# Performance work log

Measured on AMD Instinct MI355X. Metric: run time of the kernel, lower is better.

The kernel has to match this reference:

```python
import jax, jax.numpy as jnp
import numpy as np

IN_DIMS = 1024
K = 8


def setup_inputs() -> dict:
    key = jax.random.key(0)
    ks = jax.random.split(key, 7)
    s = 1.0 / np.sqrt(IN_DIMS)
    x = jax.random.normal(ks[0], (8, 2048, IN_DIMS), dtype=jnp.float32)
    Wq = jax.random.uniform(ks[1], (IN_DIMS, K), jnp.float32, -s, s)
    bq = jax.random.uniform(ks[2], (K,), jnp.float32, -s, s)
    Wk = jax.random.uniform(ks[3], (IN_DIMS, K), jnp.float32, -s, s)
    bk = jax.random.uniform(ks[4], (K,), jnp.float32, -s, s)
    Wv = jax.random.uniform(ks[5], (IN_DIMS, IN_DIMS), jnp.float32, -s, s)
    bv = jax.random.uniform(ks[6], (IN_DIMS,), jnp.float32, -s, s)
    return {"x": x, "Wq": Wq, "bq": bq, "Wk": Wk, "bk": bk, "Wv": Wv, "bv": bv}


def reference(x, Wq, bq, Wk, bk, Wv, bv):
    # x: [B,S,D]; rank-k projections
    q = jnp.einsum('bsd,dk->bsk', x, Wq) + bq        # [B,S,k]
    k = jnp.einsum('bsd,dk->bsk', x, Wk) + bk        # [B,S,k]
    energy = jnp.einsum('bik,bjk->bij', q, k)        # [B,S,S] (unscaled)
    attention = jax.nn.softmax(energy, axis=-1)
    value = jnp.einsum('bsd,de->bse', x, Wv) + bv    # [B,S,D]
    out = jnp.einsum('bij,bjd->bid', attention, value)
    return (out, attention)
```

## Files before the change

### kernel.cpp

```cpp
#include <hip/hip_runtime.h>


typedef __attribute__((ext_vector_type(8))) __bf16 bf16x8;
typedef __attribute__((ext_vector_type(4))) __bf16 bf16x4;
typedef __attribute__((ext_vector_type(4))) float  f32x4;
typedef unsigned int u32;

#define GLB_CAST(p) ((const __attribute__((address_space(1))) u32*)(p))
#define LDS_CAST(p) ((__attribute__((address_space(3))) u32*)(p))

#define S_BARRIER() { __builtin_amdgcn_s_barrier(); __builtin_amdgcn_sched_barrier(0); }
#define LGKM0()     { asm volatile("s_waitcnt lgkmcnt(0)" ::: "memory"); __builtin_amdgcn_sched_barrier(0); }
#define VMCNT8()    { asm volatile("s_waitcnt vmcnt(8)" ::: "memory"); __builtin_amdgcn_sched_barrier(0); }
#define VMCNT0()    { asm volatile("s_waitcnt vmcnt(0)" ::: "memory"); __builtin_amdgcn_sched_barrier(0); }

static constexpr int    Bn   = 8;
static constexpr int    S    = 2048;
static constexpr int    Dd   = 1024;
static constexpr int    Mtot = Bn * S;
static constexpr size_t OUT0 = (size_t)Bn * S * Dd;

static constexpr size_t OFF_XBF  = 0;
static constexpr size_t OFF_WVT  = OFF_XBF  + (size_t)Mtot * Dd * 2;
static constexpr size_t OFF_WQKT = OFF_WVT  + (size_t)Dd * Dd * 2;
static constexpr size_t OFF_Q    = OFF_WQKT + (size_t)16 * Dd * 2;
static constexpr size_t OFF_K    = OFF_Q    + (size_t)Mtot * 8 * 4;
static constexpr size_t OFF_VT   = OFF_K    + (size_t)Mtot * 8 * 4;
static constexpr size_t OFF_ATTB = OFF_VT   + (size_t)Bn * Dd * S * 2;
static constexpr size_t WS_NEED  = OFF_ATTB + (size_t)Bn * S * S * 2;

__global__ __launch_bounds__(256) void prep_kernel(
    const float* __restrict__ x, const float* __restrict__ Wq,
    const float* __restrict__ Wk, const float* __restrict__ Wv,
    __bf16* __restrict__ xbf, __bf16* __restrict__ wvt, __bf16* __restrict__ wqkT)
{
    __shared__ float lt[64][65];
    int bid = blockIdx.x, t = threadIdx.x;
    if (bid < 4096) {
        #pragma unroll
        for (int i = 0; i < 4; ++i) {
            size_t idx4 = (size_t)i * 1048576 + (size_t)bid * 256 + t;
            f32x4 v = ((const f32x4*)x)[idx4];
            bf16x4 o;
            #pragma unroll
            for (int c = 0; c < 4; ++c) o[c] = (__bf16)v[c];
            ((bf16x4*)xbf)[idx4] = o;
        }
    } else if (bid < 4352) {
        int tile = bid - 4096;
        int tr = tile >> 4, tc = tile & 15;
        int r0 = t >> 6, c = t & 63;
        #pragma unroll
        for (int i = 0; i < 16; ++i) {
            int row = i * 4 + r0;
            lt[row][c] = Wv[(size_t)(tr * 64 + row) * 1024 + tc * 64 + c];
        }
        __syncthreads();
        #pragma unroll
        for (int i = 0; i < 16; ++i) {
            int er = i * 4 + r0;
            wvt[(size_t)(tc * 64 + er) * 1024 + tr * 64 + c] = (__bf16)lt[c][er];
        }
    } else {
        int lb = bid - 4352;
        #pragma unroll
        for (int i = 0; i < 4; ++i) {
            int idx = (lb * 4 + i) * 256 + t;
            int n = idx >> 10, d = idx & 1023;
            float v = (n < 8) ? Wq[d * 8 + n] : Wk[d * 8 + (n & 7)];
            wqkT[n * 1024 + d] = (__bf16)v;
        }
    }
}

__global__ __launch_bounds__(256) void qk_proj_kernel(
    const __bf16* __restrict__ xbf, const __bf16* __restrict__ wqkT,
    const float* __restrict__ bq, const float* __restrict__ bk,
    float* __restrict__ qb, float* __restrict__ kb)
{
    int t = threadIdx.x, l = t & 63, w = t >> 6;
    int mbase = (blockIdx.x * 4 + w) * 16;
    f32x4 acc = {0.f, 0.f, 0.f, 0.f};
    const __bf16* ar = xbf + (size_t)(mbase + (l & 15)) * 1024 + ((l >> 4) << 3);
    const __bf16* br = wqkT + (size_t)(l & 15) * 1024 + ((l >> 4) << 3);
    #pragma unroll 8
    for (int kk = 0; kk < 1024; kk += 32) {
        bf16x8 a = *(const bf16x8*)(ar + kk);
        bf16x8 b = *(const bf16x8*)(br + kk);
        acc = __builtin_amdgcn_mfma_f32_16x16x32_bf16(a, b, acc, 0, 0, 0);
    }
    int n = l & 15;
    float bias = (n < 8) ? bq[n] : bk[n & 7];
    #pragma unroll
    for (int r = 0; r < 4; ++r) {
        int m = mbase + ((l >> 4) << 2) + r;
        float v = acc[r] + bias;
        if (n < 8) qb[m * 8 + n] = v;
        else       kb[m * 8 + (n & 7)] = v;
    }
}

__global__ __launch_bounds__(256) void softmax_kernel(
    const float* __restrict__ qb, const float* __restrict__ kb,
    float* __restrict__ attnF, __bf16* __restrict__ attnB)
{
    int bid = blockIdx.x;
    int b = bid >> 6, chunk = bid & 63;
    int t = threadIdx.x, l = t & 63, w = t >> 6;
    float kr[8][8];
    const float* kbb = kb + ((size_t)b << 14);
    #pragma unroll
    for (int jj = 0; jj < 8; ++jj) {
        f32x4 v0 = *(const f32x4*)(kbb + (size_t)(t * 8 + jj) * 8);
        f32x4 v1 = *(const f32x4*)(kbb + (size_t)(t * 8 + jj) * 8 + 4);
        #pragma unroll
        for (int c = 0; c < 4; ++c) { kr[jj][c] = v0[c]; kr[jj][4 + c] = v1[c]; }
    }
    __shared__ float redm[4], reds[4];
    const float* qrow = qb + ((size_t)b << 14);
    for (int ii = 0; ii < 32; ++ii) {
        int i = (chunk << 5) + ii;
        f32x4 q0 = *(const f32x4*)(qrow + (size_t)i * 8);
        f32x4 q1 = *(const f32x4*)(qrow + (size_t)i * 8 + 4);
        float e[8];
        #pragma unroll
        for (int jj = 0; jj < 8; ++jj) {
            float s = q0[0] * kr[jj][0];
            s = fmaf(q0[1], kr[jj][1], s);
            s = fmaf(q0[2], kr[jj][2], s);
            s = fmaf(q0[3], kr[jj][3], s);
            s = fmaf(q1[0], kr[jj][4], s);
            s = fmaf(q1[1], kr[jj][5], s);
            s = fmaf(q1[2], kr[jj][6], s);
            s = fmaf(q1[3], kr[jj][7], s);
            e[jj] = s;
        }
        float mx = e[0];
        #pragma unroll
        for (int jj = 1; jj < 8; ++jj) mx = fmaxf(mx, e[jj]);
        #pragma unroll
        for (int d = 1; d < 64; d <<= 1) mx = fmaxf(mx, __shfl_xor(mx, d));
        if (l == 0) redm[w] = mx;
        __syncthreads();
        mx = fmaxf(fmaxf(redm[0], redm[1]), fmaxf(redm[2], redm[3]));
        float p[8], sum = 0.f;
        #pragma unroll
        for (int jj = 0; jj < 8; ++jj) { p[jj] = __expf(e[jj] - mx); sum += p[jj]; }
        #pragma unroll
        for (int d = 1; d < 64; d <<= 1) sum += __shfl_xor(sum, d);
        if (l == 0) reds[w] = sum;
        __syncthreads();
        float T = (reds[0] + reds[1]) + (reds[2] + reds[3]);
        float inv = 1.0f / T;
        size_t off = (((size_t)b << 11) + i) * 2048 + (size_t)t * 8;
        f32x4 o0, o1; bf16x8 ob;
        #pragma unroll
        for (int c = 0; c < 4; ++c) {
            o0[c] = p[c] * inv; o1[c] = p[4 + c] * inv;
            ob[c] = (__bf16)o0[c]; ob[4 + c] = (__bf16)o1[c];
        }
        *(f32x4*)(attnF + off) = o0;
        *(f32x4*)(attnF + off + 4) = o1;
        *(bf16x8*)(attnB + off) = ob;
    }
}

template<int LDA>
__device__ __forceinline__ void stageA(const __bf16* Ab, char* smem,
    int slot, int kk, int c, int rowin, int sl8, int wid)
{
    __builtin_amdgcn_global_load_lds(
        GLB_CAST(Ab + (size_t)(c * 64 + rowin) * LDA + kk + sl8 * 8),
        LDS_CAST(smem + slot * 65536 + c * 8192 + wid * 1024), 16, 0, 0);
}
template<int LDA>
__device__ __forceinline__ void stageB(const __bf16* Bb, char* smem,
    int slot, int kk, int c, int rowin, int sl8, int wid)
{
    __builtin_amdgcn_global_load_lds(
        GLB_CAST(Bb + (size_t)(c * 64 + rowin) * LDA + kk + sl8 * 8),
        LDS_CAST(smem + slot * 65536 + 32768 + c * 8192 + wid * 1024), 16, 0, 0);
}

template<int MODE>
__global__ __launch_bounds__(512, 2) void gemm_kernel(
    const __bf16* __restrict__ A, const __bf16* __restrict__ Bt,
    float* __restrict__ outF, __bf16* __restrict__ outVt,
    const float* __restrict__ bv)
{
    constexpr int LDA = (MODE == 0) ? 1024 : 2048;
    constexpr int NT  = LDA / 64;
    __shared__ __align__(1024) char smem[131072];

    int bid = blockIdx.x;
    int wg = ((bid & 7) << 5) | (bid >> 3);
    int t = threadIdx.x, l = t & 63;
    int wid = t >> 6;
    int wmr = wid >> 2, wnc = wid & 3;

    int mblk, nblk, bb = 0;
    size_t aoff, boff;
    if constexpr (MODE == 0) {
        mblk = wg >> 2; nblk = wg & 3;
        aoff = (size_t)mblk * 256 * LDA; boff = 0;
    } else {
        bb = wg >> 5; int r = wg & 31;
        mblk = r >> 2; nblk = r & 3;
        aoff = (size_t)bb * S * S + (size_t)mblk * 256 * LDA;
        boff = (size_t)bb * Dd * S;
    }
    const __bf16* Ab = A + aoff;
    const __bf16* Bb = Bt + boff + (size_t)nblk * 256 * LDA;

    int rowin = t >> 3;
    int sl8 = (t & 7) ^ (rowin & 7);
    int lr = l & 15, lk = l >> 4;

    f32x4 acc[8][4] = {};

    #pragma unroll
    for (int c = 0; c < 4; ++c) {
        stageA<LDA>(Ab, smem, 0, 0, c, rowin, sl8, wid);
        stageB<LDA>(Bb, smem, 0, 0, c, rowin, sl8, wid);
    }
    #pragma unroll
    for (int c = 0; c < 4; ++c) {
        stageA<LDA>(Ab, smem, 1, 64, c, rowin, sl8, wid);
        stageB<LDA>(Bb, smem, 1, 64, c, rowin, sl8, wid);
    }
    VMCNT8();
    S_BARRIER();

    for (int tt = 0; tt < NT; ++tt) {
        int s = tt & 1;
        const __bf16* Asl = (const __bf16*)(smem + s * 65536);
        const __bf16* Bsl = (const __bf16*)(smem + s * 65536 + 32768);
        bool pf = (tt + 2 < NT);
        int kk2 = (tt + 2) * 64;

        bf16x8 aLo[2][4], aHi[2][4], bLo[2][2], bHi[2][2];

        #pragma unroll
        for (int ks = 0; ks < 2; ++ks) {
            int sa = ks * 4 + lk;
            #pragma unroll
            for (int i = 0; i < 4; ++i) {
                int ra = wmr * 128 + i * 16 + lr;
                aLo[ks][i] = *(const bf16x8*)&Asl[ra * 64 + ((sa ^ (ra & 7)) << 3)];
            }
            #pragma unroll
            for (int j = 0; j < 2; ++j) {
                int rb = wnc * 64 + j * 16 + lr;
                bLo[ks][j] = *(const bf16x8*)&Bsl[rb * 64 + ((sa ^ (rb & 7)) << 3)];
            }
        }
        S_BARRIER(); LGKM0();
        __builtin_amdgcn_s_setprio(1);
        #pragma unroll
        for (int ks = 0; ks < 2; ++ks)
            #pragma unroll
            for (int i = 0; i < 4; ++i)
                #pragma unroll
                for (int j = 0; j < 2; ++j)
                    acc[i][j] = __builtin_amdgcn_mfma_f32_16x16x32_bf16(aLo[ks][i], bLo[ks][j], acc[i][j], 0, 0, 0);
        __builtin_amdgcn_s_setprio(0);
        S_BARRIER();

        #pragma unroll
        for (int ks = 0; ks < 2; ++ks) {
            int sa = ks * 4 + lk;
            #pragma unroll
            for (int j = 0; j < 2; ++j) {
                int rb = wnc * 64 + (j + 2) * 16 + lr;
                bHi[ks][j] = *(const bf16x8*)&Bsl[rb * 64 + ((sa ^ (rb & 7)) << 3)];
            }
        }
        if (pf) {
            stageA<LDA>(Ab, smem, s, kk2, 0, rowin, sl8, wid);
            stageA<LDA>(Ab, smem, s, kk2, 2, rowin, sl8, wid);
        }
        S_BARRIER(); LGKM0();
        __builtin_amdgcn_s_setprio(1);
        #pragma unroll
        for (int ks = 0; ks < 2; ++ks)
            #pragma unroll
            for (int i = 0; i < 4; ++i)
                #pragma unroll
                for (int j = 0; j < 2; ++j)
                    acc[i][2 + j] = __builtin_amdgcn_mfma_f32_16x16x32_bf16(aLo[ks][i], bHi[ks][j], acc[i][2 + j], 0, 0, 0);
        __builtin_amdgcn_s_setprio(0);
        S_BARRIER();

        #pragma unroll
        for (int ks = 0; ks < 2; ++ks) {
            int sa = ks * 4 + lk;
            #pragma unroll
            for (int i = 0; i < 4; ++i) {
                int ra = wmr * 128 + (i + 4) * 16 + lr;
                aHi[ks][i] = *(const bf16x8*)&Asl[ra * 64 + ((sa ^ (ra & 7)) << 3)];
            }
        }
        if (pf) {
            #pragma unroll
            for (int c = 0; c < 4; ++c)
                stageB<LDA>(Bb, smem, s, kk2, c, rowin, sl8, wid);
        }
        S_BARRIER(); LGKM0();
        __builtin_amdgcn_s_setprio(1);
        #pragma unroll
        for (int ks = 0; ks < 2; ++ks)
            #pragma unroll
            for (int i = 0; i < 4; ++i)
                #pragma unroll
                for (int j = 0; j < 2; ++j)
                    acc[4 + i][2 + j] = __builtin_amdgcn_mfma_f32_16x16x32_bf16(aHi[ks][i], bHi[ks][j], acc[4 + i][2 + j], 0, 0, 0);
        __builtin_amdgcn_s_setprio(0);
        S_BARRIER();

        if (pf) {
            stageA<LDA>(Ab, smem, s, kk2, 1, rowin, sl8, wid);
            stageA<LDA>(Ab, smem, s, kk2, 3, rowin, sl8, wid);
        }
        S_BARRIER();
        __builtin_amdgcn_s_setprio(1);
        #pragma unroll
        for (int ks = 0; ks < 2; ++ks)
            #pragma unroll
            for (int i = 0; i < 4; ++i)
                #pragma unroll
                for (int j = 0; j < 2; ++j)
                    acc[4 + i][j] = __builtin_amdgcn_mfma_f32_16x16x32_bf16(aHi[ks][i], bLo[ks][j], acc[4 + i][j], 0, 0, 0);
        __builtin_amdgcn_s_setprio(0);

        if (tt == NT - 1) break;
        S_BARRIER();
        if (pf) { VMCNT8(); } else { VMCNT0(); }
        S_BARRIER();
    }

    if constexpr (MODE == 0) {
        #pragma unroll
        for (int j = 0; j < 4; ++j) {
            int e = (nblk << 8) + wnc * 64 + j * 16 + lr;
            float bias = bv[e];
            #pragma unroll
            for (int i = 0; i < 8; ++i) {
                int m0 = (mblk << 8) + wmr * 128 + i * 16 + (lk << 2);
                int b = m0 >> 11, s0 = m0 & 2047;
                bf16x4 o;
                #pragma unroll
                for (int r = 0; r < 4; ++r) o[r] = (__bf16)(acc[i][j][r] + bias);
                *(bf16x4*)&outVt[(((size_t)(b << 10) + e) << 11) + s0] = o;
            }
        }
    } else {
        float* ob = outF + (size_t)bb * S * Dd;
        #pragma unroll
        for (int i = 0; i < 8; ++i) {
            int m0 = (mblk << 8) + wmr * 128 + i * 16 + (lk << 2);
            #pragma unroll
            for (int j = 0; j < 4; ++j) {
                int e = (nblk << 8) + wnc * 64 + j * 16 + lr;
                #pragma unroll
                for (int r = 0; r < 4; ++r)
                    ob[(size_t)(m0 + r) * 1024 + e] = acc[i][j][r];
            }
        }
    }
}

extern "C" void kernel_launch(void* const* d_in, const int* in_sizes, int n_in,
                              void* d_out, int out_size, void* d_ws, size_t ws_size,
                              hipStream_t stream)
{
    const float* x  = (const float*)d_in[0];
    const float* Wq = (const float*)d_in[1];
    const float* bq = (const float*)d_in[2];
    const float* Wk = (const float*)d_in[3];
    const float* bk = (const float*)d_in[4];
    const float* Wv = (const float*)d_in[5];
    const float* bv = (const float*)d_in[6];

    float* outp  = (float*)d_out;
    float* attnF = outp + OUT0;

    if (ws_size < WS_NEED) return;
    char* ws = (char*)d_ws;
    __bf16* xbf   = (__bf16*)(ws + OFF_XBF);
    __bf16* wvt   = (__bf16*)(ws + OFF_WVT);
    __bf16* wqkT  = (__bf16*)(ws + OFF_WQKT);
    float*  qbuf  = (float*)(ws + OFF_Q);
    float*  kbuf  = (float*)(ws + OFF_K);
    __bf16* vt    = (__bf16*)(ws + OFF_VT);
    __bf16* attnB = (__bf16*)(ws + OFF_ATTB);

    prep_kernel<<<4368, 256, 0, stream>>>(x, Wq, Wk, Wv, xbf, wvt, wqkT);
    qk_proj_kernel<<<256, 256, 0, stream>>>(xbf, wqkT, bq, bk, qbuf, kbuf);
    gemm_kernel<0><<<256, 512, 0, stream>>>(xbf, wvt, nullptr, vt, bv);
    softmax_kernel<<<512, 256, 0, stream>>>(qbuf, kbuf, attnF, attnB);
    gemm_kernel<1><<<256, 512, 0, stream>>>(attnB, vt, outp, nullptr, nullptr);
}
```

Before: 196.3 us.

## Fuse softmax recomputation into attention-times-value GEMM, dropping bf16 attention buffer

The softmax kernel now writes only each row's max and reciprocal sum. A new fused kernel recomputes the rank-8 energies tile by tile, applies exp and normalisation, writes the fp32 attention output (from one of the two column-half blocks), and feeds bf16 probabilities through LDS into MFMA against staged V tiles. This removes the 64MB bf16 attention write and its re-read by the second GEMM. The cost is a second exp pass over the energies, a smaller tile GEMM with less reuse per block, and per-tile barriers.

```diff
diff --git a/kernel.cpp b/kernel.cpp
--- a/kernel.cpp
+++ b/kernel.cpp
@@ -12,6 +12,7 @@
 #define S_BARRIER() { __builtin_amdgcn_s_barrier(); __builtin_amdgcn_sched_barrier(0); }
 #define LGKM0()     { asm volatile("s_waitcnt lgkmcnt(0)" ::: "memory"); __builtin_amdgcn_sched_barrier(0); }
 #define VMCNT8()    { asm volatile("s_waitcnt vmcnt(8)" ::: "memory"); __builtin_amdgcn_sched_barrier(0); }
+#define VMCNT4()    { asm volatile("s_waitcnt vmcnt(4)" ::: "memory"); __builtin_amdgcn_sched_barrier(0); }
 #define VMCNT0()    { asm volatile("s_waitcnt vmcnt(0)" ::: "memory"); __builtin_amdgcn_sched_barrier(0); }
 
 static constexpr int    Bn   = 8;
@@ -26,8 +27,9 @@
 static constexpr size_t OFF_Q    = OFF_WQKT + (size_t)16 * Dd * 2;
 static constexpr size_t OFF_K    = OFF_Q    + (size_t)Mtot * 8 * 4;
 static constexpr size_t OFF_VT   = OFF_K    + (size_t)Mtot * 8 * 4;
-static constexpr size_t OFF_ATTB = OFF_VT   + (size_t)Bn * Dd * S * 2;
-static constexpr size_t WS_NEED  = OFF_ATTB + (size_t)Bn * S * S * 2;
+static constexpr size_t OFF_M    = OFF_VT   + (size_t)Bn * Dd * S * 2;
+static constexpr size_t OFF_T    = OFF_M    + (size_t)Mtot * 4;
+static constexpr size_t WS_NEED  = OFF_T    + (size_t)Mtot * 4;
 
 __global__ __launch_bounds__(256) void prep_kernel(
     const float* __restrict__ x, const float* __restrict__ Wq,
@@ -100,9 +102,9 @@
     }
 }
 
-__global__ __launch_bounds__(256) void softmax_kernel(
+__global__ __launch_bounds__(256) void mt_kernel(
     const float* __restrict__ qb, const float* __restrict__ kb,
-    float* __restrict__ attnF, __bf16* __restrict__ attnB)
+    float* __restrict__ mArr, float* __restrict__ tArr)
 {
     int bid = blockIdx.x;
     int b = bid >> 6, chunk = bid & 63;
@@ -143,25 +145,19 @@
         if (l == 0) redm[w] = mx;
         __syncthreads();
         mx = fmaxf(fmaxf(redm[0], redm[1]), fmaxf(redm[2], redm[3]));
-        float p[8], sum = 0.f;
-        #pragma unroll
-        for (int jj = 0; jj < 8; ++jj) { p[jj] = __expf(e[jj] - mx); sum += p[jj]; }
+        float sum = 0.f;
+        #pragma unroll
+        for (int jj = 0; jj < 8; ++jj) sum += __expf(e[jj] - mx);
         #pragma unroll
         for (int d = 1; d < 64; d <<= 1) sum += __shfl_xor(sum, d);
         if (l == 0) reds[w] = sum;
         __syncthreads();
         float T = (reds[0] + reds[1]) + (reds[2] + reds[3]);
-        float inv = 1.0f / T;
-        size_t off = (((size_t)b << 11) + i) * 2048 + (size_t)t * 8;
-        f32x4 o0, o1; bf16x8 ob;
-        #pragma unroll
-        for (int c = 0; c < 4; ++c) {
-            o0[c] = p[c] * inv; o1[c] = p[4 + c] * inv;
-            ob[c] = (__bf16)o0[c]; ob[4 + c] = (__bf16)o1[c];
-        }
-        *(f32x4*)(attnF + off) = o0;
-        *(f32x4*)(attnF + off + 4) = o1;
-        *(bf16x8*)(attnB + off) = ob;
+        if (t == 0) {
+            mArr[(b << 11) + i] = mx;
+            tArr[(b << 11) + i] = 1.0f / T;
+        }
+        __syncthreads();
     }
 }
 
@@ -182,13 +178,11 @@
         LDS_CAST(smem + slot * 65536 + 32768 + c * 8192 + wid * 1024), 16, 0, 0);
 }
 
-template<int MODE>
-__global__ __launch_bounds__(512, 2) void gemm_kernel(
+__global__ __launch_bounds__(512, 2) void gemm0_kernel(
     const __bf16* __restrict__ A, const __bf16* __restrict__ Bt,
-    float* __restrict__ outF, __bf16* __restrict__ outVt,
-    const float* __restrict__ bv)
-{
-    constexpr int LDA = (MODE == 0) ? 1024 : 2048;
+    __bf16* __restrict__ outVt, const float* __restrict__ bv)
+{
+    constexpr int LDA = 1024;
     constexpr int NT  = LDA / 64;
     __shared__ __align__(1024) char smem[131072];
 
@@ -198,19 +192,9 @@
     int wid = t >> 6;
     int wmr = wid >> 2, wnc = wid & 3;
 
-    int mblk, nblk, bb = 0;
-    size_t aoff, boff;
-    if constexpr (MODE == 0) {
-        mblk = wg >> 2; nblk = wg & 3;
-        aoff = (size_t)mblk * 256 * LDA; boff = 0;
-    } else {
-        bb = wg >> 5; int r = wg & 31;
-        mblk = r >> 2; nblk = r & 3;
-        aoff = (size_t)bb * S * S + (size_t)mblk * 256 * LDA;
-        boff = (size_t)bb * Dd * S;
-    }
-    const __bf16* Ab = A + aoff;
-    const __bf16* Bb = Bt + boff + (size_t)nblk * 256 * LDA;
+    int mblk = wg >> 2, nblk = wg & 3;
+    const __bf16* Ab = A + (size_t)mblk * 256 * LDA;
+    const __bf16* Bb = Bt + (size_t)nblk * 256 * LDA;
 
     int rowin = t >> 3;
     int sl8 = (t & 7) ^ (rowin & 7);
@@ -338,33 +322,144 @@
         S_BARRIER();
     }
 
-    if constexpr (MODE == 0) {
-        #pragma unroll
-        for (int j = 0; j < 4; ++j) {
-            int e = (nblk << 8) + wnc * 64 + j * 16 + lr;
-            float bias = bv[e];
-            #pragma unroll
-            for (int i = 0; i < 8; ++i) {
-                int m0 = (mblk << 8) + wmr * 128 + i * 16 + (lk << 2);
-                int b = m0 >> 11, s0 = m0 & 2047;
-                bf16x4 o;
-                #pragma unroll
-                for (int r = 0; r < 4; ++r) o[r] = (__bf16)(acc[i][j][r] + bias);
-                *(bf16x4*)&outVt[(((size_t)(b << 10) + e) << 11) + s0] = o;
-            }
-        }
-    } else {
-        float* ob = outF + (size_t)bb * S * Dd;
+    #pragma unroll
+    for (int j = 0; j < 4; ++j) {
+        int e = (nblk << 8) + wnc * 64 + j * 16 + lr;
+        float bias = bv[e];
         #pragma unroll
         for (int i = 0; i < 8; ++i) {
             int m0 = (mblk << 8) + wmr * 128 + i * 16 + (lk << 2);
-            #pragma unroll
-            for (int j = 0; j < 4; ++j) {
-                int e = (nblk << 8) + wnc * 64 + j * 16 + lr;
-                #pragma unroll
-                for (int r = 0; r < 4; ++r)
-                    ob[(size_t)(m0 + r) * 1024 + e] = acc[i][j][r];
-            }
+            int b = m0 >> 11, s0 = m0 & 2047;
+            bf16x4 o;
+            #pragma unroll
+            for (int r = 0; r < 4; ++r) o[r] = (__bf16)(acc[i][j][r] + bias);
+            *(bf16x4*)&outVt[(((size_t)(b << 10) + e) << 11) + s0] = o;
+        }
+    }
+}
+
+__device__ __forceinline__ void stageV(const __bf16* vtb, char* smem, int vs,
+    int jt0, int t, int wid)
+{
+    #pragma unroll
+    for (int u = 0; u < 4; ++u) {
+        int el = u * 128 + (t >> 2);
+        int sc = (t & 3) ^ ((el >> 1) & 3);
+        __builtin_amdgcn_global_load_lds(
+            GLB_CAST(vtb + (size_t)el * 2048 + jt0 + sc * 8),
+            LDS_CAST(smem + vs * 32768 + u * 8192 + wid * 1024), 16, 0, 0);
+    }
+}
+
+__device__ __forceinline__ void pcompute(int jt0, int ps, char* smem,
+    const float* kbb, f32x4 q0, f32x4 q1, float m, float invT,
+    float* aF, bool writeA, int pr, int jg)
+{
+    float p[8];
+    const float* kp = kbb + (size_t)(jt0 + jg * 8) * 8;
+    #pragma unroll
+    for (int jj = 0; jj < 8; ++jj) {
+        f32x4 k0 = *(const f32x4*)(kp + jj * 8);
+        f32x4 k1 = *(const f32x4*)(kp + jj * 8 + 4);
+        float s = q0[0] * k0[0];
+        s = fmaf(q0[1], k0[1], s);
+        s = fmaf(q0[2], k0[2], s);
+        s = fmaf(q0[3], k0[3], s);
+        s = fmaf(q1[0], k1[0], s);
+        s = fmaf(q1[1], k1[1], s);
+        s = fmaf(q1[2], k1[2], s);
+        s = fmaf(q1[3], k1[3], s);
+        p[jj] = __expf(s - m) * invT;
+    }
+    if (writeA) {
+        f32x4 o0 = {p[0], p[1], p[2], p[3]};
+        f32x4 o1 = {p[4], p[5], p[6], p[7]};
+        *(f32x4*)(aF + jt0 + jg * 8) = o0;
+        *(f32x4*)(aF + jt0 + jg * 8 + 4) = o1;
+    }
+    bf16x8 pb;
+    #pragma unroll
+    for (int c = 0; c < 8; ++c) pb[c] = (__bf16)p[c];
+    int sl = jg ^ ((pr >> 1) & 3);
+    *(bf16x8*)(smem + 65536 + ps * 8192 + pr * 64 + (sl << 4)) = pb;
+}
+
+__global__ __launch_bounds__(512, 2) void fused_pv_kernel(
+    const float* __restrict__ qb, const float* __restrict__ kb,
+    const float* __restrict__ mArr, const float* __restrict__ tArr,
+    const __bf16* __restrict__ vt, float* __restrict__ attnF,
+    float* __restrict__ outp)
+{
+    __shared__ __align__(1024) char smem[81920];
+    int bid = blockIdx.x;
+    int b = bid & 7, rr = bid >> 3;
+    int itile = rr >> 1, nh = rr & 1;
+    int i0 = itile * 128, e0 = nh * 512;
+    int t = threadIdx.x, l = t & 63, wid = t >> 6;
+    int lr = l & 15, lk = l >> 4;
+
+    int pr = t >> 2, jg = t & 3;
+    int grow = (b << 11) + i0 + pr;
+    const float* qrow = qb + (size_t)grow * 8;
+    f32x4 q0 = *(const f32x4*)(qrow);
+    f32x4 q1 = *(const f32x4*)(qrow + 4);
+    float m    = mArr[grow];
+    float invT = tArr[grow];
+    const float* kbb = kb + ((size_t)b << 14);
+    const __bf16* vtb = vt + (((size_t)(b << 10) + e0) << 11);
+    float* aF = attnF + ((size_t)grow << 11);
+    bool writeA = (nh == 0);
+
+    f32x4 acc[8][4] = {};
+
+    pcompute(0, 0, smem, kbb, q0, q1, m, invT, aF, writeA, pr, jg);
+    stageV(vtb, smem, 0, 0, t, wid);
+    VMCNT0(); LGKM0();
+    S_BARRIER();
+
+    for (int tt = 0; tt < 64; ++tt) {
+        int s = tt & 1;
+        if (tt < 63) {
+            pcompute((tt + 1) * 32, s ^ 1, smem, kbb, q0, q1, m, invT, aF, writeA, pr, jg);
+            stageV(vtb, smem, s ^ 1, (tt + 1) * 32, t, wid);
+            VMCNT4();
+        } else {
+            VMCNT0();
+        }
+        LGKM0();
+        S_BARRIER();
+
+        const char* Vs = smem + s * 32768;
+        const char* Ps = smem + 65536 + s * 8192;
+        bf16x8 bfr[4];
+        #pragma unroll
+        for (int eb = 0; eb < 4; ++eb) {
+            int el = wid * 64 + eb * 16 + lr;
+            bfr[eb] = *(const bf16x8*)(Vs + el * 64 + ((lk ^ ((el >> 1) & 3)) << 4));
+        }
+        __builtin_amdgcn_s_setprio(1);
+        #pragma unroll
+        for (int i = 0; i < 8; ++i) {
+            int row = i * 16 + lr;
+            bf16x8 af = *(const bf16x8*)(Ps + row * 64 + ((lk ^ ((row >> 1) & 3)) << 4));
+            #pragma unroll
+            for (int eb = 0; eb < 4; ++eb)
+                acc[i][eb] = __builtin_amdgcn_mfma_f32_16x16x32_bf16(af, bfr[eb], acc[i][eb], 0, 0, 0);
+        }
+        __builtin_amdgcn_s_setprio(0);
+        S_BARRIER();
+    }
+
+    float* ob = outp + ((size_t)b << 21);
+    #pragma unroll
+    for (int i = 0; i < 8; ++i) {
+        int m0 = i0 + i * 16 + (lk << 2);
+        #pragma unroll
+        for (int eb = 0; eb < 4; ++eb) {
+            int e = e0 + wid * 64 + eb * 16 + lr;
+            #pragma unroll
+            for (int r = 0; r < 4; ++r)
+                ob[(size_t)(m0 + r) * 1024 + e] = acc[i][eb][r];
         }
     }
 }
@@ -392,11 +487,12 @@
     float*  qbuf  = (float*)(ws + OFF_Q);
     float*  kbuf  = (float*)(ws + OFF_K);
     __bf16* vt    = (__bf16*)(ws + OFF_VT);
-    __bf16* attnB = (__bf16*)(ws + OFF_ATTB);
+    float*  mArr  = (float*)(ws + OFF_M);
+    float*  tArr  = (float*)(ws + OFF_T);
 
     prep_kernel<<<4368, 256, 0, stream>>>(x, Wq, Wk, Wv, xbf, wvt, wqkT);
     qk_proj_kernel<<<256, 256, 0, stream>>>(xbf, wqkT, bq, bk, qbuf, kbuf);
-    gemm_kernel<0><<<256, 512, 0, stream>>>(xbf, wvt, nullptr, vt, bv);
-    softmax_kernel<<<512, 256, 0, stream>>>(qbuf, kbuf, attnF, attnB);
-    gemm_kernel<1><<<256, 512, 0, stream>>>(attnB, vt, outp, nullptr, nullptr);
-}
+    mt_kernel<<<512, 256, 0, stream>>>(qbuf, kbuf, mArr, tArr);
+    gemm0_kernel<<<256, 512, 0, stream>>>(xbf, wvt, vt, bv);
+    fused_pv_kernel<<<256, 512, 0, stream>>>(qbuf, kbuf, mArr, tArr, vt, attnF, outp);
+}
```

Result: slower. 433.5 us (+120.8%).

## Fuse x bf16 conversion into Q/K projection and V GEMM, drop xbf buffer

Applied to the files above, without the earlier changes.

Removes the separate pass that converted x to a bf16 workspace copy. The Q/K projection now reads fp32 x directly inside the prep kernel, and a new dedicated V GEMM kernel loads fp32 x into registers, converts it and writes swizzled bf16 tiles to LDS with a two-stage prefetch. The V^T output is also transposed through LDS so that global stores are 16-byte contiguous. This cuts a full write and re-read of a bf16 copy of x and one kernel launch. In exchange the V GEMM reads twice as many bytes for A and does the conversion in its main loop, and its pipeline uses register loads with full vmcnt(0) waits instead of async LDS loads.

```diff
diff --git a/kernel.cpp b/kernel.cpp
--- a/kernel.cpp
+++ b/kernel.cpp
@@ -20,34 +20,50 @@
 static constexpr int    Mtot = Bn * S;
 static constexpr size_t OUT0 = (size_t)Bn * S * Dd;
 
-static constexpr size_t OFF_XBF  = 0;
-static constexpr size_t OFF_WVT  = OFF_XBF  + (size_t)Mtot * Dd * 2;
-static constexpr size_t OFF_WQKT = OFF_WVT  + (size_t)Dd * Dd * 2;
-static constexpr size_t OFF_Q    = OFF_WQKT + (size_t)16 * Dd * 2;
-static constexpr size_t OFF_K    = OFF_Q    + (size_t)Mtot * 8 * 4;
-static constexpr size_t OFF_VT   = OFF_K    + (size_t)Mtot * 8 * 4;
-static constexpr size_t OFF_ATTB = OFF_VT   + (size_t)Bn * Dd * S * 2;
+static constexpr size_t OFF_WVT  = 0;
+static constexpr size_t OFF_Q    = OFF_WVT + (size_t)Dd * Dd * 2;
+static constexpr size_t OFF_K    = OFF_Q   + (size_t)Mtot * 8 * 4;
+static constexpr size_t OFF_VT   = OFF_K   + (size_t)Mtot * 8 * 4;
+static constexpr size_t OFF_ATTB = OFF_VT  + (size_t)Bn * Dd * S * 2;
 static constexpr size_t WS_NEED  = OFF_ATTB + (size_t)Bn * S * S * 2;
 
 __global__ __launch_bounds__(256) void prep_kernel(
     const float* __restrict__ x, const float* __restrict__ Wq,
     const float* __restrict__ Wk, const float* __restrict__ Wv,
-    __bf16* __restrict__ xbf, __bf16* __restrict__ wvt, __bf16* __restrict__ wqkT)
+    const float* __restrict__ bq, const float* __restrict__ bk,
+    __bf16* __restrict__ wvt, float* __restrict__ qb, float* __restrict__ kb)
 {
     __shared__ float lt[64][65];
     int bid = blockIdx.x, t = threadIdx.x;
-    if (bid < 4096) {
-        #pragma unroll
-        for (int i = 0; i < 4; ++i) {
-            size_t idx4 = (size_t)i * 1048576 + (size_t)bid * 256 + t;
-            f32x4 v = ((const f32x4*)x)[idx4];
-            bf16x4 o;
-            #pragma unroll
-            for (int c = 0; c < 4; ++c) o[c] = (__bf16)v[c];
-            ((bf16x4*)xbf)[idx4] = o;
-        }
-    } else if (bid < 4352) {
-        int tile = bid - 4096;
+    if (bid < 256) {
+        int l = t & 63, w = t >> 6;
+        int mbase = (bid * 4 + w) * 16;
+        int n = l & 15;
+        int dbase = (l >> 4) << 3;
+        const float* xr = x + (size_t)(mbase + n) * 1024 + dbase;
+        const float* wcol = (n < 8) ? (Wq + n) : (Wk + (n & 7));
+        f32x4 acc = {0.f, 0.f, 0.f, 0.f};
+        #pragma unroll 4
+        for (int kk = 0; kk < 1024; kk += 32) {
+            f32x4 a0 = *(const f32x4*)(xr + kk);
+            f32x4 a1 = *(const f32x4*)(xr + kk + 4);
+            bf16x8 a, b;
+            #pragma unroll
+            for (int c = 0; c < 4; ++c) { a[c] = (__bf16)a0[c]; a[4 + c] = (__bf16)a1[c]; }
+            #pragma unroll
+            for (int u = 0; u < 8; ++u) b[u] = (__bf16)wcol[(size_t)(dbase + kk + u) * 8];
+            acc = __builtin_amdgcn_mfma_f32_16x16x32_bf16(a, b, acc, 0, 0, 0);
+        }
+        float bias = (n < 8) ? bq[n] : bk[n & 7];
+        #pragma unroll
+        for (int r = 0; r < 4; ++r) {
+            int m = mbase + ((l >> 4) << 2) + r;
+            float v = acc[r] + bias;
+            if (n < 8) qb[m * 8 + n] = v;
+            else       kb[m * 8 + (n & 7)] = v;
+        }
+    } else {
+        int tile = bid - 256;
         int tr = tile >> 4, tc = tile & 15;
         int r0 = t >> 6, c = t & 63;
         #pragma unroll
@@ -61,42 +77,165 @@
             int er = i * 4 + r0;
             wvt[(size_t)(tc * 64 + er) * 1024 + tr * 64 + c] = (__bf16)lt[c][er];
         }
-    } else {
-        int lb = bid - 4352;
-        #pragma unroll
-        for (int i = 0; i < 4; ++i) {
-            int idx = (lb * 4 + i) * 256 + t;
-            int n = idx >> 10, d = idx & 1023;
-            float v = (n < 8) ? Wq[d * 8 + n] : Wk[d * 8 + (n & 7)];
-            wqkT[n * 1024 + d] = (__bf16)v;
-        }
-    }
-}
-
-__global__ __launch_bounds__(256) void qk_proj_kernel(
-    const __bf16* __restrict__ xbf, const __bf16* __restrict__ wqkT,
-    const float* __restrict__ bq, const float* __restrict__ bk,
-    float* __restrict__ qb, float* __restrict__ kb)
-{
-    int t = threadIdx.x, l = t & 63, w = t >> 6;
-    int mbase = (blockIdx.x * 4 + w) * 16;
-    f32x4 acc = {0.f, 0.f, 0.f, 0.f};
-    const __bf16* ar = xbf + (size_t)(mbase + (l & 15)) * 1024 + ((l >> 4) << 3);
-    const __bf16* br = wqkT + (size_t)(l & 15) * 1024 + ((l >> 4) << 3);
-    #pragma unroll 8
-    for (int kk = 0; kk < 1024; kk += 32) {
-        bf16x8 a = *(const bf16x8*)(ar + kk);
-        bf16x8 b = *(const bf16x8*)(br + kk);
-        acc = __builtin_amdgcn_mfma_f32_16x16x32_bf16(a, b, acc, 0, 0, 0);
-    }
-    int n = l & 15;
-    float bias = (n < 8) ? bq[n] : bk[n & 7];
-    #pragma unroll
-    for (int r = 0; r < 4; ++r) {
-        int m = mbase + ((l >> 4) << 2) + r;
-        float v = acc[r] + bias;
-        if (n < 8) qb[m * 8 + n] = v;
-        else       kb[m * 8 + (n & 7)] = v;
+    }
+}
+
+__global__ __launch_bounds__(512, 2) void gemm0_kernel(
+    const float* __restrict__ X, const __bf16* __restrict__ Wvt,
+    __bf16* __restrict__ outVt, const float* __restrict__ bv)
+{
+    constexpr int NT = 16;
+    __shared__ __align__(1024) char smem[131072];
+
+    int bid = blockIdx.x;
+    int wg = ((bid & 7) << 5) | (bid >> 3);
+    int t = threadIdx.x, l = t & 63, wid = t >> 6;
+    int wmr = wid >> 2, wnc = wid & 3;
+    int mblk = wg >> 2, nblk = wg & 3;
+
+    int arow = t >> 1, ahalf = t & 1;
+    const float* Ax = X + (size_t)(mblk * 256 + arow) * 1024 + ahalf * 32;
+    int awoff[4];
+    #pragma unroll
+    for (int u = 0; u < 4; ++u)
+        awoff[u] = arow * 128 + (((ahalf * 4 + u) ^ (arow & 7)) << 4);
+
+    int rowin = t >> 3;
+    int sl8 = (t & 7) ^ (rowin & 7);
+    const __bf16* gB[4];
+    #pragma unroll
+    for (int c = 0; c < 4; ++c)
+        gB[c] = Wvt + (size_t)(nblk * 256 + c * 64 + rowin) * 1024 + sl8 * 8;
+
+    int lr = l & 15, lk = l >> 4;
+    int slot0 = (lk ^ (lr & 7)) << 3;
+    int slot1 = ((lk ^ 4) ^ (lr & 7)) << 3;
+    int offA0 = (wmr * 128 + lr) * 64 + slot0;
+    int offA1 = (wmr * 128 + lr) * 64 + slot1;
+    int offB0 = (wnc * 64 + lr) * 64 + slot0;
+    int offB1 = (wnc * 64 + lr) * 64 + slot1;
+
+    f32x4 acc[8][4] = {};
+    f32x4 xr[8];
+
+    #pragma unroll
+    for (int i = 0; i < 8; ++i) xr[i] = *(const f32x4*)(Ax + 0 * 64 + i * 4);
+    VMCNT0();
+    #pragma unroll
+    for (int u = 0; u < 4; ++u) {
+        f32x4 a0 = xr[2 * u], a1 = xr[2 * u + 1];
+        bf16x8 wv_;
+        #pragma unroll
+        for (int c = 0; c < 4; ++c) { wv_[c] = (__bf16)a0[c]; wv_[4 + c] = (__bf16)a1[c]; }
+        *(bf16x8*)(smem + awoff[u]) = wv_;
+    }
+    #pragma unroll
+    for (int c = 0; c < 4; ++c)
+        __builtin_amdgcn_global_load_lds(GLB_CAST(gB[c] + 0),
+            LDS_CAST(smem + 32768 + c * 8192 + wid * 1024), 16, 0, 0);
+    #pragma unroll
+    for (int i = 0; i < 8; ++i) xr[i] = *(const f32x4*)(Ax + 1 * 64 + i * 4);
+    VMCNT0();
+    #pragma unroll
+    for (int u = 0; u < 4; ++u) {
+        f32x4 a0 = xr[2 * u], a1 = xr[2 * u + 1];
+        bf16x8 wv_;
+        #pragma unroll
+        for (int c = 0; c < 4; ++c) { wv_[c] = (__bf16)a0[c]; wv_[4 + c] = (__bf16)a1[c]; }
+        *(bf16x8*)(smem + 65536 + awoff[u]) = wv_;
+    }
+    #pragma unroll
+    for (int c = 0; c < 4; ++c)
+        __builtin_amdgcn_global_load_lds(GLB_CAST(gB[c] + 64),
+            LDS_CAST(smem + 65536 + 32768 + c * 8192 + wid * 1024), 16, 0, 0);
+    VMCNT0();
+    LGKM0();
+    S_BARRIER();
+
+    for (int tt = 0; tt < NT; ++tt) {
+        bool pf = (tt + 2 < NT);
+        if (pf) {
+            #pragma unroll
+            for (int i = 0; i < 8; ++i)
+                xr[i] = *(const f32x4*)(Ax + (tt + 2) * 64 + i * 4);
+            __builtin_amdgcn_sched_barrier(0);
+        }
+        const __bf16* Asl = (const __bf16*)(smem + ((tt & 1) << 16));
+        const __bf16* Bsl = Asl + 16384;
+        bf16x8 af[8], bfr[4];
+        #pragma unroll
+        for (int i = 0; i < 8; ++i) af[i] = *(const bf16x8*)(Asl + offA0 + i * 1024);
+        #pragma unroll
+        for (int j = 0; j < 4; ++j) bfr[j] = *(const bf16x8*)(Bsl + offB0 + j * 1024);
+        __builtin_amdgcn_s_setprio(1);
+        #pragma unroll
+        for (int i = 0; i < 8; ++i)
+            #pragma unroll
+            for (int j = 0; j < 4; ++j)
+                acc[i][j] = __builtin_amdgcn_mfma_f32_16x16x32_bf16(af[i], bfr[j], acc[i][j], 0, 0, 0);
+        __builtin_amdgcn_s_setprio(0);
+        #pragma unroll
+        for (int i = 0; i < 8; ++i) af[i] = *(const bf16x8*)(Asl + offA1 + i * 1024);
+        #pragma unroll
+        for (int j = 0; j < 4; ++j) bfr[j] = *(const bf16x8*)(Bsl + offB1 + j * 1024);
+        __builtin_amdgcn_s_setprio(1);
+        #pragma unroll
+        for (int i = 0; i < 8; ++i)
+            #pragma unroll
+            for (int j = 0; j < 4; ++j)
+                acc[i][j] = __builtin_amdgcn_mfma_f32_16x16x32_bf16(af[i], bfr[j], acc[i][j], 0, 0, 0);
+        __builtin_amdgcn_s_setprio(0);
+
+        if (tt == NT - 1) break;
+        S_BARRIER();
+        VMCNT0();
+        if (pf) {
+            char* dst = smem + ((tt & 1) << 16);
+            #pragma unroll
+            for (int u = 0; u < 4; ++u) {
+                f32x4 a0 = xr[2 * u], a1 = xr[2 * u + 1];
+                bf16x8 wv_;
+                #pragma unroll
+                for (int c = 0; c < 4; ++c) { wv_[c] = (__bf16)a0[c]; wv_[4 + c] = (__bf16)a1[c]; }
+                *(bf16x8*)(dst + awoff[u]) = wv_;
+            }
+            #pragma unroll
+            for (int c = 0; c < 4; ++c)
+                __builtin_amdgcn_global_load_lds(GLB_CAST(gB[c] + (tt + 2) * 64),
+                    LDS_CAST(dst + 32768 + c * 8192 + wid * 1024), 16, 0, 0);
+            LGKM0();
+        }
+        S_BARRIER();
+    }
+
+    S_BARRIER();
+    #pragma unroll
+    for (int j = 0; j < 4; ++j) {
+        int e_loc = wnc * 64 + j * 16 + lr;
+        float bias = bv[(nblk << 8) + e_loc];
+        #pragma unroll
+        for (int i = 0; i < 8; ++i) {
+            int slot = wmr * 16 + i * 2 + (lk >> 1);
+            bf16x4 o;
+            #pragma unroll
+            for (int r = 0; r < 4; ++r) o[r] = (__bf16)(acc[i][j][r] + bias);
+            *(bf16x4*)(smem + e_loc * 512 + ((slot ^ (e_loc & 7)) << 4) + (lk & 1) * 8) = o;
+        }
+    }
+    S_BARRIER();
+    int b = mblk >> 3, sbase = (mblk & 7) << 8;
+    #pragma unroll
+    for (int u = 0; u < 4; ++u) {
+        int e_loc = u * 64 + (t >> 3);
+        int e_glob = (nblk << 8) + e_loc;
+        __bf16* dstp = outVt + (((size_t)(b << 10) + e_glob) << 11) + sbase;
+        int sv = t & 7;
+        #pragma unroll
+        for (int v = 0; v < 4; ++v) {
+            int svv = v * 8 + sv;
+            bf16x8 val = *(const bf16x8*)(smem + e_loc * 512 + ((svv ^ (e_loc & 7)) << 4));
+            *(bf16x8*)(dstp + svv * 8) = val;
+        }
     }
 }
 
@@ -165,31 +304,26 @@
     }
 }
 
-template<int LDA>
-__device__ __forceinline__ void stageA(const __bf16* Ab, char* smem,
+__device__ __forceinline__ void g1_stageA(const __bf16* Ab, char* smem,
     int slot, int kk, int c, int rowin, int sl8, int wid)
 {
     __builtin_amdgcn_global_load_lds(
-        GLB_CAST(Ab + (size_t)(c * 64 + rowin) * LDA + kk + sl8 * 8),
+        GLB_CAST(Ab + (size_t)(c * 64 + rowin) * 2048 + kk + sl8 * 8),
         LDS_CAST(smem + slot * 65536 + c * 8192 + wid * 1024), 16, 0, 0);
 }
-template<int LDA>
-__device__ __forceinline__ void stageB(const __bf16* Bb, char* smem,
+__device__ __forceinline__ void g1_stageB(const __bf16* Bb, char* smem,
     int slot, int kk, int c, int rowin, int sl8, int wid)
 {
     __builtin_amdgcn_global_load_lds(
-        GLB_CAST(Bb + (size_t)(c * 64 + rowin) * LDA + kk + sl8 * 8),
+        GLB_CAST(Bb + (size_t)(c * 64 + rowin) * 2048 + kk + sl8 * 8),
         LDS_CAST(smem + slot * 65536 + 32768 + c * 8192 + wid * 1024), 16, 0, 0);
 }
 
-template<int MODE>
-__global__ __launch_bounds__(512, 2) void gemm_kernel(
+__global__ __launch_bounds__(512, 2) void gemm1_kernel(
     const __bf16* __restrict__ A, const __bf16* __restrict__ Bt,
-    float* __restrict__ outF, __bf16* __restrict__ outVt,
-    const float* __restrict__ bv)
-{
-    constexpr int LDA = (MODE == 0) ? 1024 : 2048;
-    constexpr int NT  = LDA / 64;
+    float* __restrict__ outF)
+{
+    constexpr int NT = 32;
     __shared__ __align__(1024) char smem[131072];
 
     int bid = blockIdx.x;
@@ -198,19 +332,10 @@
     int wid = t >> 6;
     int wmr = wid >> 2, wnc = wid & 3;
 
-    int mblk, nblk, bb = 0;
-    size_t aoff, boff;
-    if constexpr (MODE == 0) {
-        mblk = wg >> 2; nblk = wg & 3;
-        aoff = (size_t)mblk * 256 * LDA; boff = 0;
-    } else {
-        bb = wg >> 5; int r = wg & 31;
-        mblk = r >> 2; nblk = r & 3;
-        aoff = (size_t)bb * S * S + (size_t)mblk * 256 * LDA;
-        boff = (size_t)bb * Dd * S;
-    }
-    const __bf16* Ab = A + aoff;
-    const __bf16* Bb = Bt + boff + (size_t)nblk * 256 * LDA;
+    int bb = wg >> 5; int r = wg & 31;
+    int mblk = r >> 2, nblk = r & 3;
+    const __bf16* Ab = A + (size_t)bb * S * S + (size_t)mblk * 256 * 2048;
+    const __bf16* Bb = Bt + (size_t)bb * Dd * S + (size_t)nblk * 256 * 2048;
 
     int rowin = t >> 3;
     int sl8 = (t & 7) ^ (rowin & 7);
@@ -220,13 +345,13 @@
 
     #pragma unroll
     for (int c = 0; c < 4; ++c) {
-        stageA<LDA>(Ab, smem, 0, 0, c, rowin, sl8, wid);
-        stageB<LDA>(Bb, smem, 0, 0, c, rowin, sl8, wid);
+        g1_stageA(Ab, smem, 0, 0, c, rowin, sl8, wid);
+        g1_stageB(Bb, smem, 0, 0, c, rowin, sl8, wid);
     }
     #pragma unroll
     for (int c = 0; c < 4; ++c) {
-        stageA<LDA>(Ab, smem, 1, 64, c, rowin, sl8, wid);
-        stageB<LDA>(Bb, smem, 1, 64, c, rowin, sl8, wid);
+        g1_stageA(Ab, smem, 1, 64, c, rowin, sl8, wid);
+        g1_stageB(Bb, smem, 1, 64, c, rowin, sl8, wid);
     }
     VMCNT8();
     S_BARRIER();
@@ -276,8 +401,8 @@
             }
         }
         if (pf) {
-            stageA<LDA>(Ab, smem, s, kk2, 0, rowin, sl8, wid);
-            stageA<LDA>(Ab, smem, s, kk2, 2, rowin, sl8, wid);
+            g1_stageA(Ab, smem, s, kk2, 0, rowin, sl8, wid);
+            g1_stageA(Ab, smem, s, kk2, 2, rowin, sl8, wid);
         }
         S_BARRIER(); LGKM0();
         __builtin_amdgcn_s_setprio(1);
@@ -303,7 +428,7 @@
         if (pf) {
             #pragma unroll
             for (int c = 0; c < 4; ++c)
-                stageB<LDA>(Bb, smem, s, kk2, c, rowin, sl8, wid);
+                g1_stageB(Bb, smem, s, kk2, c, rowin, sl8, wid);
         }
         S_BARRIER(); LGKM0();
         __builtin_amdgcn_s_setprio(1);
@@ -318,8 +443,8 @@
         S_BARRIER();
 
         if (pf) {
-            stageA<LDA>(Ab, smem, s, kk2, 1, rowin, sl8, wid);
-            stageA<LDA>(Ab, smem, s, kk2, 3, rowin, sl8, wid);
+            g1_stageA(Ab, smem, s, kk2, 1, rowin, sl8, wid);
+            g1_stageA(Ab, smem, s, kk2, 3, rowin, sl8, wid);
         }
         S_BARRIER();
         __builtin_amdgcn_s_setprio(1);
@@ -338,33 +463,16 @@
         S_BARRIER();
     }
 
-    if constexpr (MODE == 0) {
+    float* ob = outF + (size_t)bb * S * Dd;
+    #pragma unroll
+    for (int i = 0; i < 8; ++i) {
+        int m0 = (mblk << 8) + wmr * 128 + i * 16 + (lk << 2);
         #pragma unroll
         for (int j = 0; j < 4; ++j) {
             int e = (nblk << 8) + wnc * 64 + j * 16 + lr;
-            float bias = bv[e];
-            #pragma unroll
-            for (int i = 0; i < 8; ++i) {
-                int m0 = (mblk << 8) + wmr * 128 + i * 16 + (lk << 2);
-                int b = m0 >> 11, s0 = m0 & 2047;
-                bf16x4 o;
-                #pragma unroll
-                for (int r = 0; r < 4; ++r) o[r] = (__bf16)(acc[i][j][r] + bias);
-                *(bf16x4*)&outVt[(((size_t)(b << 10) + e) << 11) + s0] = o;
-            }
-        }
-    } else {
-        float* ob = outF + (size_t)bb * S * Dd;
-        #pragma unroll
-        for (int i = 0; i < 8; ++i) {
-            int m0 = (mblk << 8) + wmr * 128 + i * 16 + (lk << 2);
-            #pragma unroll
-            for (int j = 0; j < 4; ++j) {
-                int e = (nblk << 8) + wnc * 64 + j * 16 + lr;
-                #pragma unroll
-                for (int r = 0; r < 4; ++r)
-                    ob[(size_t)(m0 + r) * 1024 + e] = acc[i][j][r];
-            }
+            #pragma unroll
+            for (int r = 0; r < 4; ++r)
+                ob[(size_t)(m0 + r) * 1024 + e] = acc[i][j][r];
         }
     }
 }
@@ -386,17 +494,14 @@
 
     if (ws_size < WS_NEED) return;
     char* ws = (char*)d_ws;
-    __bf16* xbf   = (__bf16*)(ws + OFF_XBF);
     __bf16* wvt   = (__bf16*)(ws + OFF_WVT);
-    __bf16* wqkT  = (__bf16*)(ws + OFF_WQKT);
     float*  qbuf  = (float*)(ws + OFF_Q);
     float*  kbuf  = (float*)(ws + OFF_K);
     __bf16* vt    = (__bf16*)(ws + OFF_VT);
     __bf16* attnB = (__bf16*)(ws + OFF_ATTB);
 
-    prep_kernel<<<4368, 256, 0, stream>>>(x, Wq, Wk, Wv, xbf, wvt, wqkT);
-    qk_proj_kernel<<<256, 256, 0, stream>>>(xbf, wqkT, bq, bk, qbuf, kbuf);
-    gemm_kernel<0><<<256, 512, 0, stream>>>(xbf, wvt, nullptr, vt, bv);
+    prep_kernel<<<512, 256, 0, stream>>>(x, Wq, Wk, Wv, bq, bk, wvt, qbuf, kbuf);
+    gemm0_kernel<<<256, 512, 0, stream>>>(x, wvt, vt, bv);
     softmax_kernel<<<512, 256, 0, stream>>>(qbuf, kbuf, attnF, attnB);
-    gemm_kernel<1><<<256, 512, 0, stream>>>(attnB, vt, outp, nullptr, nullptr);
-}
+    gemm1_kernel<<<256, 512, 0, stream>>>(attnB, vt, outp);
+}
```

Measured after the change: 200.8 us. +2.3%, slower.
